# Kernel optimization log

Measured on AMD Instinct MI355X. Metric: run time of the kernel, lower is better.

## Reference

```python
import jax, jax.numpy as jnp
import numpy as np

D_MODEL = 1024
D_INNER = 2048
D_STATE = 16
D_CONV = 4
DT_RANK = 64
BATCH = 2
SEQLEN = 1024


def setup_inputs() -> dict:
    key = jax.random.key(0)
    ks = jax.random.split(key, 12)
    s = 0.02
    # dt bias initialized as inverse-softplus of dt ~ LogUniform(1e-3, 1e-1), as in the torch code
    dt = jnp.exp(jax.random.uniform(ks[7], (D_INNER,)) * (np.log(0.1) - np.log(0.001)) + np.log(0.001))
    dt = jnp.clip(dt, 1e-4, None)
    inv_dt = jnp.log(jnp.expm1(dt))
    A_log = jnp.log(jnp.broadcast_to(jnp.arange(1, D_STATE + 1, dtype=jnp.float32), (D_INNER, D_STATE)))
    return {
        "hidden_states": jax.random.normal(ks[0], (BATCH, SEQLEN, D_MODEL), jnp.float32),
        "x_text": jax.random.normal(ks[1], (BATCH, D_MODEL), jnp.float32),
        "in_proj_w": jax.random.normal(ks[2], (2 * D_INNER, D_MODEL), jnp.float32) * s,
        "conv_w": jax.random.normal(ks[3], (D_INNER, 1, D_CONV), jnp.float32) * s,
        "conv_b": jax.random.normal(ks[4], (D_INNER,), jnp.float32) * s,
        "x_proj_w": jax.random.normal(ks[5], (DT_RANK + 2 * D_STATE, D_INNER), jnp.float32) * s,
        "dt_proj_w": jax.random.normal(ks[6], (D_INNER, DT_RANK), jnp.float32) * (DT_RANK ** -0.5),
        "dt_proj_b": inv_dt.astype(jnp.float32),
        "A_log": A_log.astype(jnp.float32),
        "D": jnp.ones((D_INNER,), jnp.float32),
        "out_proj_w": jax.random.normal(ks[8], (D_MODEL, D_INNER), jnp.float32) * s,
        "gate_w": jax.random.normal(ks[9], (DT_RANK + 2 * D_STATE, D_MODEL), jnp.float32) * s,
        "gate_b": jnp.zeros((DT_RANK + 2 * D_STATE,), jnp.float32),
    }


def _causal_depthwise_conv(x, w, b):
    # x: (b, d, l), w: (d, 1, k) depthwise, left-pad k-1 for causality
    y = jax.lax.conv_general_dilated(
        x, w, window_strides=(1,), padding=[(D_CONV - 1, 0)],
        dimension_numbers=("NCH", "OIH", "NCH"), feature_group_count=D_INNER)
    return y + b[None, :, None]


def _mamba_forward(hidden_states, x_text, in_proj_w, conv_w, conv_b, x_proj_w,
                   dt_proj_w, dt_proj_b, A_log, D, out_proj_w, gate_w, gate_b):
    b = hidden_states.shape[0]
    # input projection -> x, z each (b, l, d_inner)
    xz = jnp.einsum("bld,ed->ble", hidden_states, in_proj_w)
    x, z = jnp.split(xz, 2, axis=-1)
    # causal depthwise conv + SiLU
    xc = _causal_depthwise_conv(jnp.transpose(x, (0, 2, 1)), conv_w, conv_b)
    xc = jnp.transpose(jax.nn.silu(xc), (0, 2, 1))  # (b, l, d_inner)
    # x_proj -> dt/B/C, modulated by text gate
    x_dbl = jnp.einsum("bld,ed->ble", xc, x_proj_w)  # (b, l, dt_rank+2n)
    gate = jax.nn.sigmoid(x_text @ gate_w.T + gate_b)  # (b, dt_rank+2n)
    x_dbl = x_dbl * gate[:, None, :]
    dt, Bm, Cm = jnp.split(x_dbl, [DT_RANK, DT_RANK + D_STATE], axis=-1)
    delta = jax.nn.softplus(jnp.einsum("blr,dr->bld", dt, dt_proj_w) + dt_proj_b)  # (b, l, d)
    A = -jnp.exp(A_log)  # (d, n)
    dA = jnp.exp(jnp.einsum("bld,dn->bldn", delta, A))          # (b, l, d, n)
    dBx = jnp.einsum("bld,bln->bldn", delta * xc, Bm)            # (b, l, d, n)

    def step(h, inp):
        dA_t, dBx_t, C_t = inp
        h = h * dA_t + dBx_t                       # (b, d, n)
        y_t = jnp.einsum("bdn,bn->bd", h, C_t)
        return h, y_t

    h0 = jnp.zeros((b, D_INNER, D_STATE), delta.dtype)
    _, ys = jax.lax.scan(step, h0, (jnp.transpose(dA, (1, 0, 2, 3)),
                                    jnp.transpose(dBx, (1, 0, 2, 3)),
                                    jnp.transpose(Cm, (1, 0, 2))))
    y = jnp.transpose(ys, (1, 0, 2)) + D * xc      # (b, l, d_inner)
    y = y * jax.nn.silu(z)
    return jnp.einsum("bld,md->blm", y, out_proj_w)


def reference(hidden_states, x_text, in_proj_w, conv_w, conv_b, x_proj_w,
              dt_proj_w, dt_proj_b, A_log, D, out_proj_w, gate_w, gate_b):
    return _mamba_forward(hidden_states, x_text, in_proj_w, conv_w, conv_b, x_proj_w,
                          dt_proj_w, dt_proj_b, A_log, D, out_proj_w, gate_w, gate_b)
```

## Files before the change

kernel.cpp:

```cpp
#include <hip/hip_runtime.h>

#define BATCH   2
#define SEQLEN  1024
#define DMODEL  1024
#define DINNER  2048
#define DSTATE  16
#define DCONV   4
#define DTRANK  64
#define GDIM    96
#define MROWS   (BATCH*SEQLEN)

#define NCHUNK  64
#define LCHUNK  16

typedef __attribute__((ext_vector_type(8))) short bf16x8_t;
typedef __attribute__((ext_vector_type(4))) float f32x4_t;
typedef unsigned short ushort_t;

__device__ __forceinline__ unsigned short f2bf(float x) {
    union { float f; unsigned int u; } v; v.f = x;
    unsigned int r = v.u + 0x7FFFu + ((v.u >> 16) & 1u);
    return (unsigned short)(r >> 16);
}
__device__ __forceinline__ float bf2f(unsigned short h) {
    union { unsigned int u; float f; } v; v.u = ((unsigned int)h) << 16;
    return v.f;
}

#define N1 (MROWS*DMODEL)
#define N2 (2*DINNER*DMODEL)
#define N3 (GDIM*DINNER)
#define N4 (DINNER*DTRANK)
#define N5 (DMODEL*DINNER)
__global__ __launch_bounds__(256)
void cvt5_kernel(const float* __restrict__ s1, const float* __restrict__ s2,
                 const float* __restrict__ s3, const float* __restrict__ s4,
                 const float* __restrict__ s5,
                 ushort_t* o1, ushort_t* o2, ushort_t* o3, ushort_t* o4, ushort_t* o5) {
    int idx = blockIdx.x * 256 + threadIdx.x;
    const float* src; ushort_t* dst;
    if (idx < N1)              { src = s1; dst = o1; }
    else if ((idx -= N1) < N2) { src = s2; dst = o2; }
    else if ((idx -= N2) < N3) { src = s3; dst = o3; }
    else if ((idx -= N3) < N4) { src = s4; dst = o4; }
    else if ((idx -= N4) < N5) { src = s5; dst = o5; }
    else return;
    dst[idx] = f2bf(src[idx]);
}

template<int EPI>
__global__ __launch_bounds__(256)
void gemm_bf(const ushort_t* __restrict__ A, const ushort_t* __restrict__ W,
             void* __restrict__ out0, void* __restrict__ out1,
             const float* __restrict__ bias, int M, int N, int K) {
    __shared__ __align__(16) short As[128][40];
    __shared__ __align__(16) short Bs[128][40];

    const int tid  = threadIdx.x;
    const int m0   = blockIdx.x * 128;
    const int n0   = blockIdx.y * 128;
    const int klen = K / gridDim.z;
    const int kbeg = blockIdx.z * klen;

    const int srow = tid >> 1;
    const int sseg = (tid & 1) * 16;
    const int w    = tid >> 6;
    const int lane = tid & 63;
    const int quad = lane >> 4;
    const int l15  = lane & 15;
    const int wm   = (w >> 1) * 64;
    const int wn   = (w & 1) * 64;

    f32x4_t acc[4][4];
    #pragma unroll
    for (int i = 0; i < 4; i++)
        #pragma unroll
        for (int j = 0; j < 4; j++)
            acc[i][j] = (f32x4_t){0.f, 0.f, 0.f, 0.f};

    const int arow = m0 + srow;
    const int brow = n0 + srow;
    const bool bval = (brow < N);

    for (int k0 = 0; k0 < klen; k0 += 32) {
        const int kk = kbeg + k0 + sseg;
        size_t ao = (size_t)arow * K + kk;
        bf16x8_t a0 = *(const bf16x8_t*)(A + ao);
        bf16x8_t a1 = *(const bf16x8_t*)(A + ao + 8);
        bf16x8_t b0, b1;
        if (bval) {
            size_t bo = (size_t)brow * K + kk;
            b0 = *(const bf16x8_t*)(W + bo);
            b1 = *(const bf16x8_t*)(W + bo + 8);
        } else {
            #pragma unroll
            for (int j = 0; j < 8; j++) { b0[j] = 0; b1[j] = 0; }
        }

        __syncthreads();
        *(bf16x8_t*)(&As[srow][sseg])     = a0;
        *(bf16x8_t*)(&As[srow][sseg + 8]) = a1;
        *(bf16x8_t*)(&Bs[srow][sseg])     = b0;
        *(bf16x8_t*)(&Bs[srow][sseg + 8]) = b1;
        __syncthreads();

        bf16x8_t af[4], bf[4];
        #pragma unroll
        for (int mi = 0; mi < 4; mi++)
            af[mi] = *(const bf16x8_t*)(&As[wm + mi * 16 + l15][quad * 8]);
        #pragma unroll
        for (int ni = 0; ni < 4; ni++)
            bf[ni] = *(const bf16x8_t*)(&Bs[wn + ni * 16 + l15][quad * 8]);
        #pragma unroll
        for (int mi = 0; mi < 4; mi++)
            #pragma unroll
            for (int ni = 0; ni < 4; ni++)
                acc[mi][ni] = __builtin_amdgcn_mfma_f32_16x16x32_bf16(af[mi], bf[ni], acc[mi][ni], 0, 0, 0);
    }

    const size_t zoff = (size_t)blockIdx.z * M * N;
    #pragma unroll
    for (int mi = 0; mi < 4; mi++) {
        #pragma unroll
        for (int ni = 0; ni < 4; ni++) {
            #pragma unroll
            for (int r = 0; r < 4; r++) {
                int gm = m0 + wm + mi * 16 + quad * 4 + r;
                int gn = n0 + wn + ni * 16 + l15;
                if (gn < N) {
                    float v = acc[mi][ni][r];
                    if (EPI == 0) {
                        ((float*)out0)[zoff + (size_t)gm * N + gn] = v;
                    } else if (EPI == 1) {
                        float t = v + bias[gn];
                        float sp = (t > 20.f) ? t : log1pf(__expf(t));
                        ((ushort_t*)out0)[(size_t)gm * N + gn] = f2bf(sp);
                    } else {
                        if (gn < DINNER)
                            ((float*)out0)[(size_t)gm * DINNER + gn] = v;
                        else
                            ((float*)out1)[(size_t)gm * DINNER + (gn - DINNER)] = v;
                    }
                }
            }
        }
    }
}

#define CONVBLK ((MROWS*DINNER)/256)
__global__ __launch_bounds__(256)
void convgate_kernel(const float* __restrict__ x,
                     const float* __restrict__ cw,
                     const float* __restrict__ cb,
                     ushort_t* __restrict__ xc,
                     const float* __restrict__ xt,
                     const float* __restrict__ gw,
                     const float* __restrict__ gb,
                     float* __restrict__ gate) {
    if (blockIdx.x < CONVBLK) {
        int idx = blockIdx.x * 256 + threadIdx.x;
        int d  = idx & (DINNER - 1);
        int bl = idx >> 11;
        int l  = bl & (SEQLEN - 1);
        float acc = cb[d];
        #pragma unroll
        for (int j = 0; j < DCONV; j++) {
            int lj = l - (DCONV - 1) + j;
            if (lj >= 0)
                acc += cw[d * DCONV + j] * x[(size_t)(bl - (DCONV - 1) + j) * DINNER + d];
        }
        float v = acc / (1.f + __expf(-acc));
        xc[idx] = f2bf(v);
    } else {
        int g = blockIdx.x - CONVBLK;
        int b = g / GDIM, j = g % GDIM;
        int tid = threadIdx.x;
        float s = 0.f;
        for (int k = tid; k < DMODEL; k += 256)
            s += xt[b * DMODEL + k] * gw[j * DMODEL + k];
        #pragma unroll
        for (int o = 32; o > 0; o >>= 1) s += __shfl_down(s, o);
        __shared__ float red[4];
        if ((tid & 63) == 0) red[tid >> 6] = s;
        __syncthreads();
        if (tid == 0) {
            float t = red[0] + red[1] + red[2] + red[3] + gb[j];
            gate[b * GDIM + j] = 1.f / (1.f + __expf(-t));
        }
    }
}

__global__ void gatemul_kernel(const float* __restrict__ xp,
                               const float* __restrict__ gate,
                               ushort_t* __restrict__ dt,
                               float* __restrict__ Bm,
                               float* __restrict__ Cm) {
    int idx = blockIdx.x * 256 + threadIdx.x;
    if (idx >= MROWS * GDIM) return;
    int j  = idx % GDIM;
    int bl = idx / GDIM;
    int b  = bl >> 10;
    float v = 0.f;
    #pragma unroll
    for (int z = 0; z < 16; z++)
        v += xp[(size_t)z * MROWS * GDIM + idx];
    v *= gate[b * GDIM + j];
    if (j < DTRANK)               dt[bl * DTRANK + j] = f2bf(v);
    else if (j < DTRANK + DSTATE) Bm[bl * DSTATE + (j - DTRANK)] = v;
    else                          Cm[bl * DSTATE + (j - DTRANK - DSTATE)] = v;
}

__global__ __launch_bounds__(256)
void scan1_kernel(const ushort_t* __restrict__ delta,
                  const ushort_t* __restrict__ xc,
                  const float* __restrict__ Bm,
                  const float* __restrict__ A_log,
                  float* __restrict__ hfin,
                  float* __restrict__ aprod) {
    __shared__ float sBm[LCHUNK][DSTATE];
    int tid = threadIdx.x;
    int d = blockIdx.x * 256 + tid;
    int b = blockIdx.y;
    int c = blockIdx.z;
    int l0 = c * LCHUNK;
    for (int t = tid; t < LCHUNK * DSTATE; t += 256)
        sBm[t >> 4][t & 15] = Bm[((size_t)(b * SEQLEN + l0 + (t >> 4))) * DSTATE + (t & 15)];
    __syncthreads();

    float Ac[DSTATE];
    #pragma unroll
    for (int n = 0; n < DSTATE; n++)
        Ac[n] = -__expf(A_log[d * DSTATE + n]);
    float h[DSTATE], p[DSTATE];
    #pragma unroll
    for (int n = 0; n < DSTATE; n++) { h[n] = 0.f; p[n] = 1.f; }

    for (int s = 0; s < LCHUNK; s++) {
        size_t ix = (size_t)(b * SEQLEN + l0 + s) * DINNER + d;
        float dv = bf2f(delta[ix]);
        float xv = bf2f(xc[ix]);
        float dx = dv * xv;
        #pragma unroll
        for (int n = 0; n < DSTATE; n++) {
            float e = __expf(dv * Ac[n]);
            h[n] = h[n] * e + dx * sBm[s][n];
            p[n] *= e;
        }
    }
    size_t base = ((size_t)(b * DINNER + d) * NCHUNK + c) * DSTATE;
    #pragma unroll
    for (int n = 0; n < DSTATE; n++) { hfin[base + n] = h[n]; aprod[base + n] = p[n]; }
}

__global__ __launch_bounds__(256)
void scan2_kernel(float* __restrict__ hfin,
                  const float* __restrict__ aprod) {
    int t  = blockIdx.x * 256 + threadIdx.x;
    int n  = t & 15;
    int bd = t >> 4;
    size_t base = (size_t)bd * NCHUNK * DSTATE + n;
    float H = 0.f;
    #pragma unroll 4
    for (int c = 0; c < NCHUNK; c++) {
        size_t ix = base + (size_t)c * DSTATE;
        float hl = hfin[ix];
        float p  = aprod[ix];
        hfin[ix] = H;
        H = fmaf(p, H, hl);
    }
}

__global__ __launch_bounds__(256)
void scan3_kernel(const ushort_t* __restrict__ delta,
                  ushort_t* __restrict__ xc,
                  const float* __restrict__ z,
                  const float* __restrict__ Bm,
                  const float* __restrict__ Cm,
                  const float* __restrict__ A_log,
                  const float* __restrict__ Dp,
                  const float* __restrict__ h0) {
    __shared__ float sBm[LCHUNK][DSTATE];
    __shared__ float sCm[LCHUNK][DSTATE];
    int tid = threadIdx.x;
    int d = blockIdx.x * 256 + tid;
    int b = blockIdx.y;
    int c = blockIdx.z;
    int l0 = c * LCHUNK;
    for (int t = tid; t < LCHUNK * DSTATE; t += 256) {
        size_t src = ((size_t)(b * SEQLEN + l0 + (t >> 4))) * DSTATE + (t & 15);
        sBm[t >> 4][t & 15] = Bm[src];
        sCm[t >> 4][t & 15] = Cm[src];
    }
    __syncthreads();

    float Ac[DSTATE];
    #pragma unroll
    for (int n = 0; n < DSTATE; n++)
        Ac[n] = -__expf(A_log[d * DSTATE + n]);

    float h[DSTATE];
    size_t hb0 = ((size_t)(b * DINNER + d) * NCHUNK + c) * DSTATE;
    #pragma unroll
    for (int n = 0; n < DSTATE; n++) h[n] = h0[hb0 + n];

    float Dv = Dp[d];

    for (int s = 0; s < LCHUNK; s++) {
        size_t ix = (size_t)(b * SEQLEN + l0 + s) * DINNER + d;
        float dv = bf2f(delta[ix]);
        float xv = bf2f(xc[ix]);
        float dx = dv * xv;
        float y = 0.f;
        #pragma unroll
        for (int n = 0; n < DSTATE; n++) {
            float e = __expf(dv * Ac[n]);
            h[n] = h[n] * e + dx * sBm[s][n];
            y += h[n] * sCm[s][n];
        }
        float zv = z[ix];
        float o = (y + Dv * xv) * (zv / (1.f + __expf(-zv)));
        xc[ix] = f2bf(o);
    }
}

__global__ void reduce4_kernel(const float* __restrict__ p, float* __restrict__ out, int n) {
    int i = blockIdx.x * 256 + threadIdx.x;
    if (i < n)
        out[i] = (p[i] + p[(size_t)n + i]) + (p[2 * (size_t)n + i] + p[3 * (size_t)n + i]);
}

extern "C" void kernel_launch(void* const* d_in, const int* in_sizes, int n_in,
                              void* d_out, int out_size, void* d_ws, size_t ws_size,
                              hipStream_t stream) {
    const float* hidden   = (const float*)d_in[0];
    const float* x_text   = (const float*)d_in[1];
    const float* in_proj  = (const float*)d_in[2];
    const float* conv_w   = (const float*)d_in[3];
    const float* conv_b   = (const float*)d_in[4];
    const float* x_proj   = (const float*)d_in[5];
    const float* dt_proj  = (const float*)d_in[6];
    const float* dt_bias  = (const float*)d_in[7];
    const float* A_log    = (const float*)d_in[8];
    const float* Dparam   = (const float*)d_in[9];
    const float* out_proj = (const float*)d_in[10];
    const float* gate_w   = (const float*)d_in[11];
    const float* gate_b   = (const float*)d_in[12];

    char* ws = (char*)d_ws;
    size_t off = 0;
    auto alloc = [&](size_t bytes) -> char* {
        char* p = ws + off;
        off += (bytes + 255) & ~(size_t)255;
        return p;
    };
    ushort_t* hb    = (ushort_t*)alloc((size_t)N1 * 2);
    ushort_t* w_in  = (ushort_t*)alloc((size_t)N2 * 2);
    ushort_t* w_x   = (ushort_t*)alloc((size_t)N3 * 2);
    ushort_t* w_dt  = (ushort_t*)alloc((size_t)N4 * 2);
    ushort_t* w_o   = (ushort_t*)alloc((size_t)N5 * 2);
    float*    X     = (float*)alloc((size_t)MROWS * DINNER * 4);
    float*    zbuf  = (float*)alloc((size_t)MROWS * DINNER * 4);
    float*    hfin  = (float*)alloc((size_t)BATCH * DINNER * NCHUNK * DSTATE * 4);
    float*    aprod = (float*)alloc((size_t)BATCH * DINNER * NCHUNK * DSTATE * 4);
    float*    gate  = (float*)alloc((size_t)BATCH * GDIM * 4);
    float*    Bm    = (float*)alloc((size_t)MROWS * DSTATE * 4);
    float*    Cm    = (float*)alloc((size_t)MROWS * DSTATE * 4);
    ushort_t* dt    = (ushort_t*)alloc((size_t)MROWS * DTRANK * 2);

    ushort_t* xc     = w_in;
    float*    xdbl_p = X;
    ushort_t* delta  = (ushort_t*)X;
    float*    outp   = X;

    cvt5_kernel<<<(N1 + N2 + N3 + N4 + N5 + 255) / 256, 256, 0, stream>>>(
        hidden, in_proj, x_proj, dt_proj, out_proj, hb, w_in, w_x, w_dt, w_o);

    gemm_bf<3><<<dim3(MROWS / 128, (2 * DINNER) / 128, 1), 256, 0, stream>>>(
        hb, w_in, X, zbuf, nullptr, MROWS, 2 * DINNER, DMODEL);

    convgate_kernel<<<CONVBLK + BATCH * GDIM, 256, 0, stream>>>(
        X, conv_w, conv_b, xc, x_text, gate_w, gate_b, gate);

    gemm_bf<0><<<dim3(MROWS / 128, 1, 16), 256, 0, stream>>>(
        xc, w_x, xdbl_p, nullptr, nullptr, MROWS, GDIM, DINNER);

    gatemul_kernel<<<(MROWS * GDIM + 255) / 256, 256, 0, stream>>>(
        xdbl_p, gate, dt, Bm, Cm);

    gemm_bf<1><<<dim3(MROWS / 128, DINNER / 128, 1), 256, 0, stream>>>(
        dt, w_dt, delta, nullptr, dt_bias, MROWS, DINNER, DTRANK);

    scan1_kernel<<<dim3(DINNER / 256, BATCH, NCHUNK), 256, 0, stream>>>(
        delta, xc, Bm, A_log, hfin, aprod);

    scan2_kernel<<<(BATCH * DINNER * DSTATE) / 256, 256, 0, stream>>>(hfin, aprod);

    scan3_kernel<<<dim3(DINNER / 256, BATCH, NCHUNK), 256, 0, stream>>>(
        delta, xc, zbuf, Bm, Cm, A_log, Dparam, hfin);

    gemm_bf<0><<<dim3(MROWS / 128, DMODEL / 128, 4), 256, 0, stream>>>(
        xc, w_o, outp, nullptr, nullptr, MROWS, DMODEL, DINNER);

    reduce4_kernel<<<(MROWS * DMODEL + 255) / 256, 256, 0, stream>>>(
        outp, (float*)d_out, MROWS * DMODEL);
}
```

Baseline: 298.6 us.

## Use direct global-to-LDS loads in GEMM, vectorize convert, parallelize chunk-state scan

```diff
diff --git a/kernel.cpp b/kernel.cpp
--- a/kernel.cpp
+++ b/kernel.cpp
@@ -12,9 +12,11 @@
 
 #define NCHUNK  64
 #define LCHUNK  16
+#define SPLITX  32
 
 typedef __attribute__((ext_vector_type(8))) short bf16x8_t;
 typedef __attribute__((ext_vector_type(4))) float f32x4_t;
+typedef __attribute__((ext_vector_type(4))) unsigned short u16x4_t;
 typedef unsigned short ushort_t;
 
 __device__ __forceinline__ unsigned short f2bf(float x) {
@@ -25,6 +27,12 @@
 __device__ __forceinline__ float bf2f(unsigned short h) {
     union { unsigned int u; float f; } v; v.u = ((unsigned int)h) << 16;
     return v.f;
+}
+
+__device__ __forceinline__ void gload_lds16(const ushort_t* g, short* l) {
+    __builtin_amdgcn_global_load_lds(
+        (const __attribute__((address_space(1))) unsigned int*)g,
+        (__attribute__((address_space(3))) unsigned int*)l, 16, 0, 0);
 }
 
 #define N1 (MROWS*DMODEL)
@@ -32,20 +40,25 @@
 #define N3 (GDIM*DINNER)
 #define N4 (DINNER*DTRANK)
 #define N5 (DMODEL*DINNER)
+#define NTOT (N1+N2+N3+N4+N5)
 __global__ __launch_bounds__(256)
 void cvt5_kernel(const float* __restrict__ s1, const float* __restrict__ s2,
                  const float* __restrict__ s3, const float* __restrict__ s4,
                  const float* __restrict__ s5,
                  ushort_t* o1, ushort_t* o2, ushort_t* o3, ushort_t* o4, ushort_t* o5) {
-    int idx = blockIdx.x * 256 + threadIdx.x;
+    int idx = (blockIdx.x * 256 + threadIdx.x) * 4;
+    if (idx >= NTOT) return;
     const float* src; ushort_t* dst;
     if (idx < N1)              { src = s1; dst = o1; }
     else if ((idx -= N1) < N2) { src = s2; dst = o2; }
     else if ((idx -= N2) < N3) { src = s3; dst = o3; }
     else if ((idx -= N3) < N4) { src = s4; dst = o4; }
-    else if ((idx -= N4) < N5) { src = s5; dst = o5; }
-    else return;
-    dst[idx] = f2bf(src[idx]);
+    else                       { idx -= N4; src = s5; dst = o5; }
+    f32x4_t v = *(const f32x4_t*)(src + idx);
+    u16x4_t o;
+    #pragma unroll
+    for (int j = 0; j < 4; j++) o[j] = f2bf(v[j]);
+    *(u16x4_t*)(dst + idx) = o;
 }
 
 template<int EPI>
@@ -53,8 +66,8 @@
 void gemm_bf(const ushort_t* __restrict__ A, const ushort_t* __restrict__ W,
              void* __restrict__ out0, void* __restrict__ out1,
              const float* __restrict__ bias, int M, int N, int K) {
-    __shared__ __align__(16) short As[128][40];
-    __shared__ __align__(16) short Bs[128][40];
+    __shared__ __align__(16) short As[128 * 32];
+    __shared__ __align__(16) short Bs[128 * 32];
 
     const int tid  = threadIdx.x;
     const int m0   = blockIdx.x * 128;
@@ -62,8 +75,6 @@
     const int klen = K / gridDim.z;
     const int kbeg = blockIdx.z * klen;
 
-    const int srow = tid >> 1;
-    const int sseg = (tid & 1) * 16;
     const int w    = tid >> 6;
     const int lane = tid & 63;
     const int quad = lane >> 4;
@@ -71,6 +82,14 @@
     const int wm   = (w >> 1) * 64;
     const int wn   = (w & 1) * 64;
 
+    const int rA0 = (w * 2 + 0) * 16 + (lane >> 2);
+    const int rA1 = (w * 2 + 1) * 16 + (lane >> 2);
+    const int kc  = (lane & 3) * 8;
+    const int arow0 = m0 + rA0;
+    const int arow1 = m0 + rA1;
+    int brow0 = n0 + rA0; if (brow0 > N - 1) brow0 = N - 1;
+    int brow1 = n0 + rA1; if (brow1 > N - 1) brow1 = N - 1;
+
     f32x4_t acc[4][4];
     #pragma unroll
     for (int i = 0; i < 4; i++)
@@ -78,44 +97,27 @@
         for (int j = 0; j < 4; j++)
             acc[i][j] = (f32x4_t){0.f, 0.f, 0.f, 0.f};
 
-    const int arow = m0 + srow;
-    const int brow = n0 + srow;
-    const bool bval = (brow < N);
-
     for (int k0 = 0; k0 < klen; k0 += 32) {
-        const int kk = kbeg + k0 + sseg;
-        size_t ao = (size_t)arow * K + kk;
-        bf16x8_t a0 = *(const bf16x8_t*)(A + ao);
-        bf16x8_t a1 = *(const bf16x8_t*)(A + ao + 8);
-        bf16x8_t b0, b1;
-        if (bval) {
-            size_t bo = (size_t)brow * K + kk;
-            b0 = *(const bf16x8_t*)(W + bo);
-            b1 = *(const bf16x8_t*)(W + bo + 8);
-        } else {
-            #pragma unroll
-            for (int j = 0; j < 8; j++) { b0[j] = 0; b1[j] = 0; }
-        }
-
+        const int kk = kbeg + k0 + kc;
         __syncthreads();
-        *(bf16x8_t*)(&As[srow][sseg])     = a0;
-        *(bf16x8_t*)(&As[srow][sseg + 8]) = a1;
-        *(bf16x8_t*)(&Bs[srow][sseg])     = b0;
-        *(bf16x8_t*)(&Bs[srow][sseg + 8]) = b1;
+        gload_lds16(A + (size_t)arow0 * K + kk, &As[(w * 2 + 0) * 512]);
+        gload_lds16(A + (size_t)arow1 * K + kk, &As[(w * 2 + 1) * 512]);
+        gload_lds16(W + (size_t)brow0 * K + kk, &Bs[(w * 2 + 0) * 512]);
+        gload_lds16(W + (size_t)brow1 * K + kk, &Bs[(w * 2 + 1) * 512]);
         __syncthreads();
 
-        bf16x8_t af[4], bf[4];
+        bf16x8_t af[4], bfv[4];
         #pragma unroll
         for (int mi = 0; mi < 4; mi++)
-            af[mi] = *(const bf16x8_t*)(&As[wm + mi * 16 + l15][quad * 8]);
+            af[mi] = *(const bf16x8_t*)(&As[(wm + mi * 16 + l15) * 32 + quad * 8]);
         #pragma unroll
         for (int ni = 0; ni < 4; ni++)
-            bf[ni] = *(const bf16x8_t*)(&Bs[wn + ni * 16 + l15][quad * 8]);
+            bfv[ni] = *(const bf16x8_t*)(&Bs[(wn + ni * 16 + l15) * 32 + quad * 8]);
         #pragma unroll
         for (int mi = 0; mi < 4; mi++)
             #pragma unroll
             for (int ni = 0; ni < 4; ni++)
-                acc[mi][ni] = __builtin_amdgcn_mfma_f32_16x16x32_bf16(af[mi], bf[ni], acc[mi][ni], 0, 0, 0);
+                acc[mi][ni] = __builtin_amdgcn_mfma_f32_16x16x32_bf16(af[mi], bfv[ni], acc[mi][ni], 0, 0, 0);
     }
 
     const size_t zoff = (size_t)blockIdx.z * M * N;
@@ -202,7 +204,7 @@
     int b  = bl >> 10;
     float v = 0.f;
     #pragma unroll
-    for (int z = 0; z < 16; z++)
+    for (int z = 0; z < SPLITX; z++)
         v += xp[(size_t)z * MROWS * GDIM + idx];
     v *= gate[b * GDIM + j];
     if (j < DTRANK)               dt[bl * DTRANK + j] = f2bf(v);
@@ -255,18 +257,39 @@
 __global__ __launch_bounds__(256)
 void scan2_kernel(float* __restrict__ hfin,
                   const float* __restrict__ aprod) {
-    int t  = blockIdx.x * 256 + threadIdx.x;
-    int n  = t & 15;
-    int bd = t >> 4;
-    size_t base = (size_t)bd * NCHUNK * DSTATE + n;
-    float H = 0.f;
-    #pragma unroll 4
-    for (int c = 0; c < NCHUNK; c++) {
-        size_t ix = base + (size_t)c * DSTATE;
-        float hl = hfin[ix];
-        float p  = aprod[ix];
-        hfin[ix] = H;
-        H = fmaf(p, H, hl);
+    __shared__ float sh[NCHUNK * DSTATE];
+    __shared__ float sp[NCHUNK * DSTATE];
+    const int tid = threadIdx.x;
+    const size_t base = (size_t)blockIdx.x * (NCHUNK * DSTATE);
+    #pragma unroll
+    for (int r = 0; r < 4; r++) {
+        int i = tid + r * 256;
+        sh[i] = hfin[base + i];
+        sp[i] = aprod[base + i];
+    }
+    __syncthreads();
+    #pragma unroll
+    for (int s = 1; s < NCHUNK; s <<= 1) {
+        float nh[4], np[4];
+        #pragma unroll
+        for (int r = 0; r < 4; r++) {
+            int i = tid + r * 256;
+            int c = i >> 4;
+            if (c >= s) {
+                int j = i - (s << 4);
+                nh[r] = sh[i] + sp[i] * sh[j];
+                np[r] = sp[i] * sp[j];
+            } else { nh[r] = sh[i]; np[r] = sp[i]; }
+        }
+        __syncthreads();
+        #pragma unroll
+        for (int r = 0; r < 4; r++) { int i = tid + r * 256; sh[i] = nh[r]; sp[i] = np[r]; }
+        __syncthreads();
+    }
+    #pragma unroll
+    for (int r = 0; r < 4; r++) {
+        int i = tid + r * 256;
+        hfin[base + i] = (i >> 4) ? sh[i - 16] : 0.f;
     }
 }
 
@@ -368,11 +391,11 @@
     ushort_t* dt    = (ushort_t*)alloc((size_t)MROWS * DTRANK * 2);
 
     ushort_t* xc     = w_in;
-    float*    xdbl_p = X;
+    float*    xdbl_p = hfin;
     ushort_t* delta  = (ushort_t*)X;
     float*    outp   = X;
 
-    cvt5_kernel<<<(N1 + N2 + N3 + N4 + N5 + 255) / 256, 256, 0, stream>>>(
+    cvt5_kernel<<<(NTOT / 4 + 255) / 256, 256, 0, stream>>>(
         hidden, in_proj, x_proj, dt_proj, out_proj, hb, w_in, w_x, w_dt, w_o);
 
     gemm_bf<3><<<dim3(MROWS / 128, (2 * DINNER) / 128, 1), 256, 0, stream>>>(
@@ -381,7 +404,7 @@
     convgate_kernel<<<CONVBLK + BATCH * GDIM, 256, 0, stream>>>(
         X, conv_w, conv_b, xc, x_text, gate_w, gate_b, gate);
 
-    gemm_bf<0><<<dim3(MROWS / 128, 1, 16), 256, 0, stream>>>(
+    gemm_bf<0><<<dim3(MROWS / 128, 1, SPLITX), 256, 0, stream>>>(
         xc, w_x, xdbl_p, nullptr, nullptr, MROWS, GDIM, DINNER);
 
     gatemul_kernel<<<(MROWS * GDIM + 255) / 256, 256, 0, stream>>>(
@@ -393,7 +416,7 @@
     scan1_kernel<<<dim3(DINNER / 256, BATCH, NCHUNK), 256, 0, stream>>>(
         delta, xc, Bm, A_log, hfin, aprod);
 
-    scan2_kernel<<<(BATCH * DINNER * DSTATE) / 256, 256, 0, stream>>>(hfin, aprod);
+    scan2_kernel<<<BATCH * DINNER, 256, 0, stream>>>(hfin, aprod);
 
     scan3_kernel<<<dim3(DINNER / 256, BATCH, NCHUNK), 256, 0, stream>>>(
         delta, xc, zbuf, Bm, Cm, A_log, Dparam, hfin);
```

Result: no change. 293.8 us (-1.6%).
